# Optimization experiments

Measured on AMD Instinct MI355X. Metric: run time of the kernel, lower is better.

Reference implementation:

```python
import jax, jax.numpy as jnp
import numpy as np
from jax import lax

EPS_BN = 1e-5
EPS_LN = 1e-5


def setup_inputs() -> dict:
    key = jax.random.key(0)
    ks = jax.random.split(key, 10)
    B, Cin, H, W = 32, 512, 56, 56
    Cout, Cr = 128, 128 // 16  # CBAM reduction 16
    x = jax.random.normal(ks[0], (B, Cin, H, W), dtype=jnp.float32)
    w_proj = jax.random.normal(ks[1], (Cout, Cin), dtype=jnp.float32) * 0.02
    bn_g = jnp.ones((Cout,), jnp.float32)
    bn_b = jnp.zeros((Cout,), jnp.float32)
    bn_m = jax.random.normal(ks[2], (Cout,), dtype=jnp.float32) * 0.1
    bn_v = jax.random.uniform(ks[3], (Cout,), dtype=jnp.float32, minval=0.5, maxval=1.5)
    ca_w1 = jax.random.normal(ks[4], (Cr, Cout), dtype=jnp.float32) * 0.05
    ca_w2 = jax.random.normal(ks[5], (Cout, Cr), dtype=jnp.float32) * 0.05
    sa_w = jax.random.normal(ks[6], (1, 2, 7, 7), dtype=jnp.float32) * 0.05
    ln_g = jnp.ones((Cout,), jnp.float32)
    ln_b = jnp.zeros((Cout,), jnp.float32)
    return dict(x=x, w_proj=w_proj, bn_g=bn_g, bn_b=bn_b, bn_m=bn_m, bn_v=bn_v,
                ca_w1=ca_w1, ca_w2=ca_w2, sa_w=sa_w, ln_g=ln_g, ln_b=ln_b)


def _cbam(x, ca_w1, ca_w2, sa_w):
    # Channel attention: shared MLP on GAP and GMP over spatial dims
    avg = x.mean(axis=(2, 3))  # [B, C]
    mx = x.max(axis=(2, 3))    # [B, C]
    mlp = lambda p: jnp.einsum('cr,br->bc', ca_w2, jax.nn.relu(jnp.einsum('rc,bc->br', ca_w1, p)))
    ca = jax.nn.sigmoid(mlp(avg) + mlp(mx))  # [B, C]
    x = x * ca[:, :, None, None]
    # Spatial attention: channel-wise avg/max -> 7x7 conv -> sigmoid
    s = jnp.stack([x.mean(axis=1), x.max(axis=1)], axis=1)  # [B, 2, H, W]
    sa = lax.conv_general_dilated(s, sa_w, (1, 1), [(3, 3), (3, 3)],
                                  dimension_numbers=('NCHW', 'OIHW', 'NCHW'))
    return x * jax.nn.sigmoid(sa)


def reference(x, w_proj, bn_g, bn_b, bn_m, bn_v, ca_w1, ca_w2, sa_w, ln_g, ln_b):
    # 1x1 conv (no bias) as GEMM over channels
    h = jnp.einsum('bchw,oc->bohw', x, w_proj)
    # BatchNorm (inference) + SiLU
    scale = (bn_g / jnp.sqrt(bn_v + EPS_BN))[None, :, None, None]
    shift = (bn_b - bn_m * bn_g / jnp.sqrt(bn_v + EPS_BN))[None, :, None, None]
    h = h * scale + shift
    h = h * jax.nn.sigmoid(h)  # SiLU
    # CBAM with residual
    y = _cbam(h, ca_w1, ca_w2, sa_w) + h
    # GAP over spatial -> LayerNorm over channels
    y = y.mean(axis=(2, 3))  # [B, C]
    mu = y.mean(axis=-1, keepdims=True)
    var = ((y - mu) ** 2).mean(axis=-1, keepdims=True)
    return (y - mu) / jnp.sqrt(var + EPS_LN) * ln_g + ln_b
```

## Files before the change

### kernel.cpp

```cpp
#include <hip/hip_runtime.h>
#include <hip/hip_bf16.h>

typedef __bf16 bf16x8 __attribute__((ext_vector_type(8)));
typedef float f32x4 __attribute__((ext_vector_type(4)));

#define NB 32
#define CIN 512
#define COUT 128
#define NP 3136
#define WIMG 56

__device__ __forceinline__ unsigned fenc(float f) {
    unsigned u = __float_as_uint(f);
    return (u & 0x80000000u) ? ~u : (u | 0x80000000u);
}
__device__ __forceinline__ float fdec(unsigned e) {
    unsigned u = (e & 0x80000000u) ? (e ^ 0x80000000u) : ~e;
    return __uint_as_float(u);
}
__device__ __forceinline__ float bflo(unsigned u) { return __uint_as_float(u << 16); }
__device__ __forceinline__ float bfhi(unsigned u) { return __uint_as_float(u & 0xffff0000u); }

__device__ __forceinline__ void lds_barrier() {
    asm volatile("s_waitcnt lgkmcnt(0)" ::: "memory");
    __builtin_amdgcn_s_barrier();
    __builtin_amdgcn_sched_barrier(0);
}

__global__ __launch_bounds__(256) void k_wcvt(const float* __restrict__ wp,
                                              ushort* __restrict__ wb,
                                              unsigned* __restrict__ zero8k)
{
    int i = blockIdx.x * 256 + threadIdx.x;
    if (i < 2 * NB * COUT) zero8k[i] = 0u;
    float4 f = *(const float4*)(wp + i * 4);
    ushort4 u;
    __bf16 b0 = (__bf16)f.x, b1 = (__bf16)f.y, b2 = (__bf16)f.z, b3 = (__bf16)f.w;
    u.x = *(ushort*)&b0; u.y = *(ushort*)&b1; u.z = *(ushort*)&b2; u.w = *(ushort*)&b3;
    *(ushort4*)(wb + i * 4) = u;
}

__global__ __launch_bounds__(512, 4) void k_main(
    const float* __restrict__ x, const ushort* __restrict__ wb,
    const float* __restrict__ bn_g, const float* __restrict__ bn_b,
    const float* __restrict__ bn_m, const float* __restrict__ bn_v,
    ushort* __restrict__ hout, float* __restrict__ sumh, unsigned* __restrict__ mxenc)
{
    __shared__ __align__(16) ushort Xs[2][64 * 64];
    __shared__ float bnss[256];

    const int bid  = blockIdx.x;
    const int swz  = (bid & 7) * 196 + (bid >> 3);
    const int t    = threadIdx.x;
    const int b    = swz / 49;
    const int p0   = (swz % 49) * 64;
    const int lane = t & 63;
    const int l15  = lane & 15;
    const int lg   = lane >> 4;
    const int w    = t >> 6;

    if (t < COUT) {
        float sc = bn_g[t] * rsqrtf(bn_v[t] + 1e-5f);
        bnss[t]        = sc;
        bnss[t + COUT] = bn_b[t] - bn_m[t] * sc;
    }

    const ushort* wrow = wb + (w * 16 + l15) * CIN + lg * 8;
    bf16x8 af[16];
#pragma unroll
    for (int ks = 0; ks < 16; ++ks)
        af[ks] = *(const bf16x8*)(wrow + ks * 32);

    const int pr = t & 63;
    const int kg = w;
    const float* xb = x + ((size_t)b * CIN) * NP + p0 + pr;
    const int wbyte = pr * 128 + ((kg * 16) ^ ((pr & 7) << 4));

    f32x4 acc[4];
#pragma unroll
    for (int nf = 0; nf < 4; ++nf) acc[nf] = (f32x4){0.f, 0.f, 0.f, 0.f};

    float ld[2][8];

#pragma unroll
    for (int j = 0; j < 8; ++j) ld[0][j] = xb[(kg * 8 + j) * NP];
#pragma unroll
    for (int j = 0; j < 8; ++j) ld[1][j] = xb[(64 + kg * 8 + j) * NP];
    {
        bf16x8 v8;
#pragma unroll
        for (int j = 0; j < 8; ++j) v8[j] = (__bf16)ld[0][j];
        *(bf16x8*)((char*)Xs[0] + wbyte) = v8;
    }

#pragma unroll
    for (int kc = 0; kc < 8; ++kc) {
        lds_barrier();
        if (kc < 6) {
#pragma unroll
            for (int j = 0; j < 8; ++j)
                ld[kc & 1][j] = xb[((kc + 2) * 64 + kg * 8 + j) * NP];
        }
#pragma unroll
        for (int ks = 0; ks < 2; ++ks) {
#pragma unroll
            for (int nf = 0; nf < 4; ++nf) {
                int row  = nf * 16 + l15;
                int byte = row * 128 + ((ks * 64 + lg * 16) ^ ((row & 7) << 4));
                bf16x8 bfr = *(const bf16x8*)((const char*)Xs[kc & 1] + byte);
                acc[nf] = __builtin_amdgcn_mfma_f32_16x16x32_bf16(
                    af[kc * 2 + ks], bfr, acc[nf], 0, 0, 0);
            }
        }
        if (kc < 7) {
            bf16x8 v8;
#pragma unroll
            for (int j = 0; j < 8; ++j) v8[j] = (__bf16)ld[(kc + 1) & 1][j];
            *(bf16x8*)((char*)Xs[(kc + 1) & 1] + wbyte) = v8;
        }
    }

#pragma unroll
    for (int reg = 0; reg < 4; ++reg) {
        int o = w * 16 + lg * 4 + reg;
        float sc = bnss[o], sh = bnss[o + COUT];
        float s_ = 0.f, m_ = -1e30f;
#pragma unroll
        for (int nf = 0; nf < 4; ++nf) {
            float d    = acc[nf][reg];
            float hval = d * sc + sh;
            hval       = hval / (1.f + __expf(-hval));
            s_ += hval;
            m_ = fmaxf(m_, hval);
            int p      = p0 + nf * 16 + l15;
            __bf16 hb  = (__bf16)hval;
            hout[((size_t)b * COUT + o) * NP + p] = *(ushort*)&hb;
        }
#pragma unroll
        for (int d = 1; d < 16; d <<= 1) {
            s_ += __shfl_xor(s_, d, 64);
            m_ = fmaxf(m_, __shfl_xor(m_, d, 64));
        }
        if (l15 == 0) {
            atomicAdd(&sumh[b * COUT + o], s_);
            atomicMax(&mxenc[b * COUT + o], fenc(m_));
        }
    }
}

__global__ void k_ca(const float* __restrict__ sumh, const unsigned* __restrict__ mxenc,
                     const float* __restrict__ w1, const float* __restrict__ w2,
                     float* __restrict__ ca)
{
    int b = blockIdx.x, t = threadIdx.x;
    __shared__ float avg[128], mx[128], r1[16];
    avg[t] = sumh[b * COUT + t] * (1.f / (float)NP);
    mx[t]  = fdec(mxenc[b * COUT + t]);
    __syncthreads();
    if (t < 16) {
        int r = t & 7;
        const float* p = (t < 8) ? avg : mx;
        float s = 0.f;
        for (int c = 0; c < 128; ++c) s += w1[r * 128 + c] * p[c];
        r1[t] = fmaxf(s, 0.f);
    }
    __syncthreads();
    float s = 0.f;
#pragma unroll
    for (int r = 0; r < 8; ++r) s += w2[t * 8 + r] * (r1[r] + r1[r + 8]);
    ca[b * COUT + t] = 1.f / (1.f + __expf(-s));
}

__global__ __launch_bounds__(256) void k_sstat(const ushort* __restrict__ h,
                                               const float* __restrict__ ca,
                                               float* __restrict__ sbuf)
{
    int b = blockIdx.y, z = blockIdx.z;
    int pp = blockIdx.x * 256 + threadIdx.x;
    __shared__ float cas[32];
    if (threadIdx.x < 32) cas[threadIdx.x] = ca[b * COUT + z * 32 + threadIdx.x];
    __syncthreads();
    if (pp >= NP / 2) return;
    int p = pp * 2;
    const ushort* hb = h + ((size_t)b * COUT + z * 32) * NP + p;
    float s0 = 0.f, s1 = 0.f, m0 = -1e30f, m1 = -1e30f;
#pragma unroll 4
    for (int c = 0; c < 32; ++c) {
        unsigned u = *(const unsigned*)(hb + (size_t)c * NP);
        float cv = cas[c];
        float v0 = bflo(u) * cv;
        float v1 = bfhi(u) * cv;
        s0 += v0; s1 += v1;
        m0 = fmaxf(m0, v0); m1 = fmaxf(m1, v1);
    }
    float* sb = sbuf + ((size_t)(z * NB + b) * 2) * NP;
    sb[p] = s0; sb[p + 1] = s1;
    sb[NP + p] = m0; sb[NP + p + 1] = m1;
}

__global__ __launch_bounds__(256) void k_conv(const float* __restrict__ sbuf,
                                              const float* __restrict__ saw,
                                              float* __restrict__ sigsa)
{
    int band = blockIdx.x, b = blockIdx.y;
    int y0 = band * 7;
    int t = threadIdx.x;
    __shared__ float s[2][13 * WIMG];
    __shared__ float w[98];
    if (t < 98) w[t] = saw[t];
    for (int i = t; i < 13 * WIMG; i += 256) {
        int yy = y0 - 3 + i / WIMG;
        float vs = 0.f, vm = 0.f;
        if (yy >= 0 && yy < WIMG) {
            int p = yy * WIMG + (i % WIMG);
            float ssum = 0.f, smax = -1e30f;
#pragma unroll
            for (int z = 0; z < 4; ++z) {
                const float* sb = sbuf + ((size_t)(z * NB + b) * 2) * NP;
                ssum += sb[p];
                smax = fmaxf(smax, sb[NP + p]);
            }
            vs = ssum * (1.f / (float)COUT);
            vm = smax;
        }
        s[0][i] = vs;
        s[1][i] = vm;
    }
    __syncthreads();
    for (int i = t; i < 7 * WIMG; i += 256) {
        int ly = i / WIMG, px = i % WIMG;
        float a = 0.f;
#pragma unroll
        for (int ch = 0; ch < 2; ++ch) {
#pragma unroll
            for (int dy = 0; dy < 7; ++dy) {
                int li = (ly + dy) * WIMG;
                for (int dx = 0; dx < 7; ++dx) {
                    int xx = px + dx - 3;
                    if (xx < 0 || xx >= WIMG) continue;
                    a += s[ch][li + xx] * w[ch * 49 + dy * 7 + dx];
                }
            }
        }
        sigsa[b * NP + (y0 + ly) * WIMG + px] = 1.f / (1.f + __expf(-a));
    }
}

__global__ __launch_bounds__(256) void k_wsum(const ushort* __restrict__ h,
                                              const float* __restrict__ sigsa,
                                              const float* __restrict__ sumh,
                                              const float* __restrict__ ca,
                                              float* __restrict__ y)
{
    int bo = blockIdx.x;
    int b = bo >> 7;
    int t = threadIdx.x;
    const ushort* hr = h + (size_t)bo * NP;
    const float* sg  = sigsa + (size_t)b * NP;
    float s = 0.f;
#pragma unroll
    for (int i = 0; i < 3; ++i) {
        int q = (i * 256 + t) * 4;
        uint2 u = *(const uint2*)(hr + q);
        float4 g = *(const float4*)(sg + q);
        s += bflo(u.x) * g.x + bfhi(u.x) * g.y + bflo(u.y) * g.z + bfhi(u.y) * g.w;
    }
    if (t < 16) {
        int q = (768 + t) * 4;
        uint2 u = *(const uint2*)(hr + q);
        float4 g = *(const float4*)(sg + q);
        s += bflo(u.x) * g.x + bfhi(u.x) * g.y + bflo(u.y) * g.z + bfhi(u.y) * g.w;
    }
#pragma unroll
    for (int d = 1; d < 64; d <<= 1) s += __shfl_xor(s, d, 64);
    __shared__ float part[4];
    if ((t & 63) == 0) part[t >> 6] = s;
    __syncthreads();
    if (t == 0) {
        float tt = part[0] + part[1] + part[2] + part[3];
        y[bo] = (sumh[bo] + ca[bo] * tt) * (1.f / (float)NP);
    }
}

__global__ void k_ln(const float* __restrict__ y, const float* __restrict__ g,
                     const float* __restrict__ bta, float* __restrict__ out)
{
    int b = blockIdx.x, t = threadIdx.x;
    __shared__ float pr[2], pr2[2];
    float v = y[b * COUT + t];
    float s = v;
#pragma unroll
    for (int d = 1; d < 64; d <<= 1) s += __shfl_xor(s, d, 64);
    if ((t & 63) == 0) pr[t >> 6] = s;
    __syncthreads();
    float mu = (pr[0] + pr[1]) * (1.f / (float)COUT);
    float dv = v - mu;
    float q = dv * dv;
#pragma unroll
    for (int d = 1; d < 64; d <<= 1) q += __shfl_xor(q, d, 64);
    if ((t & 63) == 0) pr2[t >> 6] = q;
    __syncthreads();
    float var = (pr2[0] + pr2[1]) * (1.f / (float)COUT);
    out[b * COUT + t] = dv * rsqrtf(var + 1e-5f) * g[t] + bta[t];
}

extern "C" void kernel_launch(void* const* d_in, const int* in_sizes, int n_in,
                              void* d_out, int out_size, void* d_ws, size_t ws_size,
                              hipStream_t stream)
{
    const float* x     = (const float*)d_in[0];
    const float* wp    = (const float*)d_in[1];
    const float* bn_g  = (const float*)d_in[2];
    const float* bn_b  = (const float*)d_in[3];
    const float* bn_m  = (const float*)d_in[4];
    const float* bn_v  = (const float*)d_in[5];
    const float* ca_w1 = (const float*)d_in[6];
    const float* ca_w2 = (const float*)d_in[7];
    const float* sa_w  = (const float*)d_in[8];
    const float* ln_g  = (const float*)d_in[9];
    const float* ln_b  = (const float*)d_in[10];
    float* out = (float*)d_out;

    char* ws = (char*)d_ws;
    size_t off = 0;
    ushort*   hbuf  = (ushort*)(ws + off);   off += (size_t)NB * COUT * NP * 2;
    float*    sumh  = (float*)(ws + off);    off += NB * COUT * 4;
    unsigned* mxenc = (unsigned*)(ws + off); off += NB * COUT * 4;
    float*    ca    = (float*)(ws + off);    off += NB * COUT * 4;
    float*    sbuf  = (float*)(ws + off);    off += (size_t)4 * NB * 2 * NP * 4;
    float*    sigsa = (float*)(ws + off);    off += (size_t)NB * NP * 4;
    float*    ybuf  = (float*)(ws + off);    off += NB * COUT * 4;
    ushort*   wb16  = (ushort*)(ws + off);   off += (size_t)COUT * CIN * 2;

    k_wcvt<<<64, 256, 0, stream>>>(wp, wb16, (unsigned*)sumh);
    k_main<<<NB * 49, 512, 0, stream>>>(x, wb16, bn_g, bn_b, bn_m, bn_v, hbuf, sumh, mxenc);
    k_ca<<<NB, 128, 0, stream>>>(sumh, mxenc, ca_w1, ca_w2, ca);
    k_sstat<<<dim3(7, NB, 4), 256, 0, stream>>>(hbuf, ca, sbuf);
    k_conv<<<dim3(8, NB), 256, 0, stream>>>(sbuf, sa_w, sigsa);
    k_wsum<<<NB * COUT, 256, 0, stream>>>(hbuf, sigsa, sumh, ca, ybuf);
    k_ln<<<NB, 128, 0, stream>>>(ybuf, ln_g, ln_b, out);
}
```

Measured before the change: 89.51 us.

## Fuse channel attention, spatial attention, weighted sum and LayerNorm into one kernel

Replaces the five post-GEMM kernels with a single per-batch 1024-thread kernel that keeps channel scales, spatial statistics and the sigmoid map in shared memory. This removes four kernel launches and the global round trips through the ca, sbuf, sigsa and ybuf buffers. In exchange the tail runs as only 32 blocks, so each one streams its full batch slice of h twice with limited GPU-wide parallelism.

```diff
diff --git a/kernel.cpp b/kernel.cpp
--- a/kernel.cpp
+++ b/kernel.cpp
@@ -148,160 +148,150 @@
     }
 }
 
-__global__ void k_ca(const float* __restrict__ sumh, const unsigned* __restrict__ mxenc,
-                     const float* __restrict__ w1, const float* __restrict__ w2,
-                     float* __restrict__ ca)
+__global__ __launch_bounds__(1024) void k_tail(
+    const ushort* __restrict__ h, const float* __restrict__ sumh,
+    const unsigned* __restrict__ mxenc,
+    const float* __restrict__ w1, const float* __restrict__ w2,
+    const float* __restrict__ saw,
+    const float* __restrict__ ln_g, const float* __restrict__ ln_b,
+    float* __restrict__ out)
 {
-    int b = blockIdx.x, t = threadIdx.x;
-    __shared__ float avg[128], mx[128], r1[16];
-    avg[t] = sumh[b * COUT + t] * (1.f / (float)NP);
-    mx[t]  = fdec(mxenc[b * COUT + t]);
+    const int i = blockIdx.x;
+    const int b = (i & 7) * 4 + (i >> 3);
+    const int t = threadIdx.x;
+    const int wv = t >> 6, lane = t & 63;
+
+    __shared__ float s0[NP];
+    __shared__ float s1[NP];
+    __shared__ float sg[NP];
+    __shared__ float cas[COUT];
+    __shared__ float w[98];
+    __shared__ float r1[16];
+    __shared__ float yv[COUT];
+    __shared__ float red[4];
+
+    const ushort* hb = h + (size_t)b * COUT * NP;
+
+    if (t < 98) w[t] = saw[t];
+    if (t < COUT) {
+        s0[t] = sumh[b * COUT + t] * (1.f / (float)NP);
+        s1[t] = fdec(mxenc[b * COUT + t]);
+    }
     __syncthreads();
     if (t < 16) {
         int r = t & 7;
-        const float* p = (t < 8) ? avg : mx;
+        const float* p = (t < 8) ? s0 : s1;
         float s = 0.f;
-        for (int c = 0; c < 128; ++c) s += w1[r * 128 + c] * p[c];
+        for (int c = 0; c < COUT; ++c) s += w1[r * COUT + c] * p[c];
         r1[t] = fmaxf(s, 0.f);
     }
     __syncthreads();
-    float s = 0.f;
-#pragma unroll
-    for (int r = 0; r < 8; ++r) s += w2[t * 8 + r] * (r1[r] + r1[r + 8]);
-    ca[b * COUT + t] = 1.f / (1.f + __expf(-s));
-}
-
-__global__ __launch_bounds__(256) void k_sstat(const ushort* __restrict__ h,
-                                               const float* __restrict__ ca,
-                                               float* __restrict__ sbuf)
-{
-    int b = blockIdx.y, z = blockIdx.z;
-    int pp = blockIdx.x * 256 + threadIdx.x;
-    __shared__ float cas[32];
-    if (threadIdx.x < 32) cas[threadIdx.x] = ca[b * COUT + z * 32 + threadIdx.x];
-    __syncthreads();
-    if (pp >= NP / 2) return;
-    int p = pp * 2;
-    const ushort* hb = h + ((size_t)b * COUT + z * 32) * NP + p;
-    float s0 = 0.f, s1 = 0.f, m0 = -1e30f, m1 = -1e30f;
-#pragma unroll 4
-    for (int c = 0; c < 32; ++c) {
-        unsigned u = *(const unsigned*)(hb + (size_t)c * NP);
-        float cv = cas[c];
-        float v0 = bflo(u) * cv;
-        float v1 = bfhi(u) * cv;
-        s0 += v0; s1 += v1;
-        m0 = fmaxf(m0, v0); m1 = fmaxf(m1, v1);
-    }
-    float* sb = sbuf + ((size_t)(z * NB + b) * 2) * NP;
-    sb[p] = s0; sb[p + 1] = s1;
-    sb[NP + p] = m0; sb[NP + p + 1] = m1;
-}
-
-__global__ __launch_bounds__(256) void k_conv(const float* __restrict__ sbuf,
-                                              const float* __restrict__ saw,
-                                              float* __restrict__ sigsa)
-{
-    int band = blockIdx.x, b = blockIdx.y;
-    int y0 = band * 7;
-    int t = threadIdx.x;
-    __shared__ float s[2][13 * WIMG];
-    __shared__ float w[98];
-    if (t < 98) w[t] = saw[t];
-    for (int i = t; i < 13 * WIMG; i += 256) {
-        int yy = y0 - 3 + i / WIMG;
-        float vs = 0.f, vm = 0.f;
-        if (yy >= 0 && yy < WIMG) {
-            int p = yy * WIMG + (i % WIMG);
-            float ssum = 0.f, smax = -1e30f;
-#pragma unroll
-            for (int z = 0; z < 4; ++z) {
-                const float* sb = sbuf + ((size_t)(z * NB + b) * 2) * NP;
-                ssum += sb[p];
-                smax = fmaxf(smax, sb[NP + p]);
+    if (t < COUT) {
+        float s = 0.f;
+#pragma unroll
+        for (int r = 0; r < 8; ++r) s += w2[t * 8 + r] * (r1[r] + r1[r + 8]);
+        cas[t] = 1.f / (1.f + __expf(-s));
+    }
+    __syncthreads();
+
+    {
+        float a0 = 0.f, a1 = 0.f, m0 = -1e30f, m1 = -1e30f;
+        float a2 = 0.f, a3 = 0.f, m2 = -1e30f, m3 = -1e30f;
+        const bool two = (t + 1024) < (NP / 2);
+        for (int c = 0; c < COUT; ++c) {
+            float cv = cas[c];
+            const ushort* hr = hb + (size_t)c * NP;
+            unsigned u = *(const unsigned*)(hr + 2 * t);
+            float v0 = bflo(u) * cv, v1 = bfhi(u) * cv;
+            a0 += v0; a1 += v1;
+            m0 = fmaxf(m0, v0); m1 = fmaxf(m1, v1);
+            if (two) {
+                unsigned q = *(const unsigned*)(hr + 2 * (t + 1024));
+                float v2 = bflo(q) * cv, v3 = bfhi(q) * cv;
+                a2 += v2; a3 += v3;
+                m2 = fmaxf(m2, v2); m3 = fmaxf(m3, v3);
             }
-            vs = ssum * (1.f / (float)COUT);
-            vm = smax;
-        }
-        s[0][i] = vs;
-        s[1][i] = vm;
-    }
-    __syncthreads();
-    for (int i = t; i < 7 * WIMG; i += 256) {
-        int ly = i / WIMG, px = i % WIMG;
+        }
+        s0[2 * t]     = a0 * (1.f / (float)COUT);
+        s0[2 * t + 1] = a1 * (1.f / (float)COUT);
+        s1[2 * t]     = m0;
+        s1[2 * t + 1] = m1;
+        if (two) {
+            int p = 2 * (t + 1024);
+            s0[p]     = a2 * (1.f / (float)COUT);
+            s0[p + 1] = a3 * (1.f / (float)COUT);
+            s1[p]     = m2;
+            s1[p + 1] = m3;
+        }
+    }
+    __syncthreads();
+
+    for (int p = t; p < NP; p += 1024) {
+        int py = p / WIMG, px = p % WIMG;
         float a = 0.f;
 #pragma unroll
-        for (int ch = 0; ch < 2; ++ch) {
-#pragma unroll
-            for (int dy = 0; dy < 7; ++dy) {
-                int li = (ly + dy) * WIMG;
-                for (int dx = 0; dx < 7; ++dx) {
-                    int xx = px + dx - 3;
-                    if (xx < 0 || xx >= WIMG) continue;
-                    a += s[ch][li + xx] * w[ch * 49 + dy * 7 + dx];
-                }
+        for (int dy = 0; dy < 7; ++dy) {
+            int yy = py + dy - 3;
+            if (yy < 0 || yy >= WIMG) continue;
+            int li = yy * WIMG;
+            for (int dx = 0; dx < 7; ++dx) {
+                int xx = px + dx - 3;
+                if (xx < 0 || xx >= WIMG) continue;
+                a += s0[li + xx] * w[dy * 7 + dx] + s1[li + xx] * w[49 + dy * 7 + dx];
             }
         }
-        sigsa[b * NP + (y0 + ly) * WIMG + px] = 1.f / (1.f + __expf(-a));
-    }
-}
-
-__global__ __launch_bounds__(256) void k_wsum(const ushort* __restrict__ h,
-                                              const float* __restrict__ sigsa,
-                                              const float* __restrict__ sumh,
-                                              const float* __restrict__ ca,
-                                              float* __restrict__ y)
-{
-    int bo = blockIdx.x;
-    int b = bo >> 7;
-    int t = threadIdx.x;
-    const ushort* hr = h + (size_t)bo * NP;
-    const float* sg  = sigsa + (size_t)b * NP;
-    float s = 0.f;
-#pragma unroll
-    for (int i = 0; i < 3; ++i) {
-        int q = (i * 256 + t) * 4;
-        uint2 u = *(const uint2*)(hr + q);
-        float4 g = *(const float4*)(sg + q);
-        s += bflo(u.x) * g.x + bfhi(u.x) * g.y + bflo(u.y) * g.z + bfhi(u.y) * g.w;
-    }
-    if (t < 16) {
-        int q = (768 + t) * 4;
-        uint2 u = *(const uint2*)(hr + q);
-        float4 g = *(const float4*)(sg + q);
-        s += bflo(u.x) * g.x + bfhi(u.x) * g.y + bflo(u.y) * g.z + bfhi(u.y) * g.w;
-    }
-#pragma unroll
-    for (int d = 1; d < 64; d <<= 1) s += __shfl_xor(s, d, 64);
-    __shared__ float part[4];
-    if ((t & 63) == 0) part[t >> 6] = s;
-    __syncthreads();
-    if (t == 0) {
-        float tt = part[0] + part[1] + part[2] + part[3];
-        y[bo] = (sumh[bo] + ca[bo] * tt) * (1.f / (float)NP);
-    }
-}
-
-__global__ void k_ln(const float* __restrict__ y, const float* __restrict__ g,
-                     const float* __restrict__ bta, float* __restrict__ out)
-{
-    int b = blockIdx.x, t = threadIdx.x;
-    __shared__ float pr[2], pr2[2];
-    float v = y[b * COUT + t];
-    float s = v;
-#pragma unroll
-    for (int d = 1; d < 64; d <<= 1) s += __shfl_xor(s, d, 64);
-    if ((t & 63) == 0) pr[t >> 6] = s;
-    __syncthreads();
-    float mu = (pr[0] + pr[1]) * (1.f / (float)COUT);
-    float dv = v - mu;
-    float q = dv * dv;
-#pragma unroll
-    for (int d = 1; d < 64; d <<= 1) q += __shfl_xor(q, d, 64);
-    if ((t & 63) == 0) pr2[t >> 6] = q;
-    __syncthreads();
-    float var = (pr2[0] + pr2[1]) * (1.f / (float)COUT);
-    out[b * COUT + t] = dv * rsqrtf(var + 1e-5f) * g[t] + bta[t];
+        sg[p] = 1.f / (1.f + __expf(-a));
+    }
+    __syncthreads();
+
+#pragma unroll
+    for (int oo = 0; oo < 8; ++oo) {
+        int o = wv * 8 + oo;
+        const ushort* hr = hb + (size_t)o * NP;
+        float s = 0.f;
+#pragma unroll
+        for (int j = 0; j < 12; ++j) {
+            int q = j * 64 + lane;
+            uint2 u = *(const uint2*)(hr + 4 * q);
+            s += bflo(u.x) * sg[4 * q]     + bfhi(u.x) * sg[4 * q + 1]
+               + bflo(u.y) * sg[4 * q + 2] + bfhi(u.y) * sg[4 * q + 3];
+        }
+        if (lane < 16) {
+            int q = 768 + lane;
+            uint2 u = *(const uint2*)(hr + 4 * q);
+            s += bflo(u.x) * sg[4 * q]     + bfhi(u.x) * sg[4 * q + 1]
+               + bflo(u.y) * sg[4 * q + 2] + bfhi(u.y) * sg[4 * q + 3];
+        }
+#pragma unroll
+        for (int d = 1; d < 64; d <<= 1) s += __shfl_xor(s, d, 64);
+        if (lane == 0)
+            yv[o] = (sumh[b * COUT + o] + cas[o] * s) * (1.f / (float)NP);
+    }
+    __syncthreads();
+
+    if (t < COUT) {
+        float v = yv[t];
+        float s = v;
+#pragma unroll
+        for (int d = 1; d < 64; d <<= 1) s += __shfl_xor(s, d, 64);
+        if ((t & 63) == 0) red[t >> 6] = s;
+    }
+    __syncthreads();
+    if (t < COUT) {
+        float mu = (red[0] + red[1]) * (1.f / (float)COUT);
+        float dv = yv[t] - mu;
+        float q = dv * dv;
+#pragma unroll
+        for (int d = 1; d < 64; d <<= 1) q += __shfl_xor(q, d, 64);
+        if ((t & 63) == 0) red[2 + (t >> 6)] = q;
+    }
+    __syncthreads();
+    if (t < COUT) {
+        float mu  = (red[0] + red[1]) * (1.f / (float)COUT);
+        float var = (red[2] + red[3]) * (1.f / (float)COUT);
+        float dv  = yv[t] - mu;
+        out[b * COUT + t] = dv * rsqrtf(var + 1e-5f) * ln_g[t] + ln_b[t];
+    }
 }
 
 extern "C" void kernel_launch(void* const* d_in, const int* in_sizes, int n_in,
@@ -326,17 +316,9 @@
     ushort*   hbuf  = (ushort*)(ws + off);   off += (size_t)NB * COUT * NP * 2;
     float*    sumh  = (float*)(ws + off);    off += NB * COUT * 4;
     unsigned* mxenc = (unsigned*)(ws + off); off += NB * COUT * 4;
-    float*    ca    = (float*)(ws + off);    off += NB * COUT * 4;
-    float*    sbuf  = (float*)(ws + off);    off += (size_t)4 * NB * 2 * NP * 4;
-    float*    sigsa = (float*)(ws + off);    off += (size_t)NB * NP * 4;
-    float*    ybuf  = (float*)(ws + off);    off += NB * COUT * 4;
     ushort*   wb16  = (ushort*)(ws + off);   off += (size_t)COUT * CIN * 2;
 
     k_wcvt<<<64, 256, 0, stream>>>(wp, wb16, (unsigned*)sumh);
     k_main<<<NB * 49, 512, 0, stream>>>(x, wb16, bn_g, bn_b, bn_m, bn_v, hbuf, sumh, mxenc);
-    k_ca<<<NB, 128, 0, stream>>>(sumh, mxenc, ca_w1, ca_w2, ca);
-    k_sstat<<<dim3(7, NB, 4), 256, 0, stream>>>(hbuf, ca, sbuf);
-    k_conv<<<dim3(8, NB), 256, 0, stream>>>(sbuf, sa_w, sigsa);
-    k_wsum<<<NB * COUT, 256, 0, stream>>>(hbuf, sigsa, sumh, ca, ybuf);
-    k_ln<<<NB, 128, 0, stream>>>(ybuf, ln_g, ln_b, out);
-}
+    k_tail<<<NB, 1024, 0, stream>>>(hbuf, sumh, mxenc, ca_w1, ca_w2, sa_w, ln_g, ln_b, out);
+}
```

New measurement: 136.8 us. 1.53x slower.
